# Optimization experiments

Measured on AMD Instinct MI355X. Metric: run time of the kernel, lower is better.

## Reference

```python
import jax, jax.numpy as jnp
import numpy as np


def setup_inputs() -> dict:
    key = jax.random.key(0)
    kY, kH = jax.random.split(key)
    B, M, L, S = 4, 512, 31, 2
    W = M + L - 1  # 542: dispersed measurement width
    Y = jax.random.uniform(kY, (B, M, W, S), dtype=jnp.float32)
    H = jax.random.uniform(kH, (B, M, M, L), dtype=jnp.float32)
    return {"Y": Y, "H": H}


def reference(Y, H):
    # Y: [B, M, W, S] measurement (W = M+L-1), H: [B, M, M, L] coded aperture
    B, M, W, S = Y.shape
    L = H.shape[-1]
    # tf.roll(Y, -i, axis=2)[:, :, 0:M] == Y[:, :, (j+i) % W] for j in [0, M)
    idx = (jnp.arange(M)[:, None] + jnp.arange(L)[None, :]) % W  # [M, L]
    Xs = Y[:, :, idx, :]                      # [B, M, M, L, S] shifted volume
    X = jnp.sum(H[..., None] * Xs, axis=4)    # sum over shots -> [B, M, M, L]
    return X / jnp.max(X)
```

## Files before the change

kernel.cpp:

```cpp
#include <hip/hip_runtime.h>

#define CB 4
#define CM 512
#define CL 31
#define CW 542
#define SLAB  (CM * CL)
#define SLAB4 (SLAB / 4)
#define NBM   (CB * CM)
#define CPAD  543


__device__ __forceinline__ void stage_ysum(const float* __restrict__ Y, int bm,
                                           float* __restrict__ ys) {
    const float2* y2 = (const float2*)(Y + (size_t)bm * (CW * 2));
    for (int j = threadIdx.x; j < CW; j += 256) {
        float2 v = y2[j];
        float s = v.x + v.y;
        ys[j]            = s;
        ys[j + CPAD]     = s;
        ys[j + 2 * CPAD] = s;
        ys[j + 3 * CPAD] = s;
    }
}

struct IdxState {
    int l0;
    int i0;
};

__device__ __forceinline__ IdxState idx_init(int tid) {
    unsigned f = 4u * (unsigned)tid;
    unsigned n = f / 31u;
    IdxState s;
    s.l0 = (int)(f - n * 31u);
    s.i0 = (int)n + s.l0;
    return s;
}

__device__ __forceinline__ void idx_quad(const IdxState& s,
                                         int& i0, int& i1, int& i2, int& i3) {
    i0 = s.i0;
    i1 = s.i0 + ((s.l0 >= 30) ? 1 - 30 : 1);
    i2 = s.i0 + ((s.l0 >= 29) ? 2 - 30 : 2);
    i3 = s.i0 + ((s.l0 >= 28) ? 3 - 30 : 3);
}

__device__ __forceinline__ void idx_step(IdxState& s) {
    bool w = (s.l0 == 30);
    s.i0 += w ? 4 : 34;
    s.l0  = w ? 0 : (s.l0 + 1);
}

__global__ __launch_bounds__(256, 8) void cassi_max(
    const float* __restrict__ Y,
    const float* __restrict__ H,
    float* __restrict__ blockmax)
{
    __shared__ float ysum[4 * CPAD];
    __shared__ float smax[4];
    const int bm  = blockIdx.x;
    const int tid = threadIdx.x;

    stage_ysum(Y, bm, ysum);
    __syncthreads();

    const float* ys = ysum + ((tid >> 3) & 3) * CPAD;
    const float4* h4 = (const float4*)(H + (size_t)bm * SLAB);

    IdxState st = idx_init(tid);
    float mx = 0.0f;

#pragma unroll 5
    for (int k = 0; k < 15; ++k) {
        float4 h = h4[tid + (k << 8)];
        int i0, i1, i2, i3;
        idx_quad(st, i0, i1, i2, i3);
        float v0 = h.x * ys[i0];
        float v1 = h.y * ys[i1];
        float v2 = h.z * ys[i2];
        float v3 = h.w * ys[i3];
        mx = fmaxf(mx, fmaxf(fmaxf(v0, v1), fmaxf(v2, v3)));
        idx_step(st);
    }
    if (tid < 128) {
        float4 h = h4[tid + 15 * 256];
        int i0, i1, i2, i3;
        idx_quad(st, i0, i1, i2, i3);
        float v0 = h.x * ys[i0];
        float v1 = h.y * ys[i1];
        float v2 = h.z * ys[i2];
        float v3 = h.w * ys[i3];
        mx = fmaxf(mx, fmaxf(fmaxf(v0, v1), fmaxf(v2, v3)));
    }

#pragma unroll
    for (int off = 32; off > 0; off >>= 1)
        mx = fmaxf(mx, __shfl_down(mx, off, 64));
    if ((tid & 63) == 0) smax[tid >> 6] = mx;
    __syncthreads();
    if (tid == 0)
        blockmax[bm] = fmaxf(fmaxf(smax[0], smax[1]), fmaxf(smax[2], smax[3]));
}

__global__ __launch_bounds__(256, 8) void cassi_out(
    const float* __restrict__ Y,
    const float* __restrict__ H,
    const float* __restrict__ blockmax,
    float* __restrict__ out)
{
    __shared__ float ysum[4 * CPAD];
    __shared__ float sm[4];
    const int bm  = blockIdx.x;
    const int tid = threadIdx.x;

    stage_ysum(Y, bm, ysum);

    float m = 0.0f;
    for (int j = tid; j < NBM; j += 256) m = fmaxf(m, blockmax[j]);
#pragma unroll
    for (int off = 32; off > 0; off >>= 1)
        m = fmaxf(m, __shfl_down(m, off, 64));
    if ((tid & 63) == 0) sm[tid >> 6] = m;
    __syncthreads();
    const float inv = 1.0f / fmaxf(fmaxf(sm[0], sm[1]), fmaxf(sm[2], sm[3]));

    const float* ys = ysum + ((tid >> 3) & 3) * CPAD;
    const float4* h4 = (const float4*)(H + (size_t)bm * SLAB);
    float4* o4 = (float4*)(out + (size_t)bm * SLAB);

    IdxState st = idx_init(tid);

#pragma unroll 5
    for (int k = 0; k < 15; ++k) {
        float4 h = h4[tid + (k << 8)];
        int i0, i1, i2, i3;
        idx_quad(st, i0, i1, i2, i3);
        float4 o;
        o.x = h.x * ys[i0] * inv;
        o.y = h.y * ys[i1] * inv;
        o.z = h.z * ys[i2] * inv;
        o.w = h.w * ys[i3] * inv;
        o4[tid + (k << 8)] = o;
        idx_step(st);
    }
    if (tid < 128) {
        float4 h = h4[tid + 15 * 256];
        int i0, i1, i2, i3;
        idx_quad(st, i0, i1, i2, i3);
        float4 o;
        o.x = h.x * ys[i0] * inv;
        o.y = h.y * ys[i1] * inv;
        o.z = h.z * ys[i2] * inv;
        o.w = h.w * ys[i3] * inv;
        o4[tid + 15 * 256] = o;
    }
}

extern "C" void kernel_launch(void* const* d_in, const int* in_sizes, int n_in,
                              void* d_out, int out_size, void* d_ws, size_t ws_size,
                              hipStream_t stream)
{
    const float* Y = (const float*)d_in[0];
    const float* H = (const float*)d_in[1];
    float* out = (float*)d_out;
    float* blockmax = (float*)d_ws;

    cassi_max<<<NBM, 256, 0, stream>>>(Y, H, blockmax);
    cassi_out<<<NBM, 256, 0, stream>>>(Y, H, blockmax, out);
}
```

Baseline: 259.5 us.

## Fuse max and scale passes into one cooperative kernel with grid sync

Merges the two launches into one cooperative kernel. Each block computes its slab max, a grid-wide sync makes every block max visible, and the block then rescales its own slab, keeping Y staging and possibly H in cache between phases. The second pass also uses nontemporal loads and stores. If the cooperative launch fails, it falls back to the two-kernel path. Risks are the cost of the grid barrier and the launch failing because 2048 blocks must all be resident at once.

```diff
diff --git a/kernel.cpp b/kernel.cpp
--- a/kernel.cpp
+++ b/kernel.cpp
@@ -1,4 +1,7 @@
 #include <hip/hip_runtime.h>
+#include <hip/hip_cooperative_groups.h>
+
+namespace cg = cooperative_groups;
 
 #define CB 4
 #define CM 512
@@ -8,6 +11,8 @@
 #define SLAB4 (SLAB / 4)
 #define NBM   (CB * CM)
 #define CPAD  543
+
+typedef float f32x4 __attribute__((ext_vector_type(4)));
 
 
 __device__ __forceinline__ void stage_ysum(const float* __restrict__ Y, int bm,
@@ -51,10 +56,74 @@
     s.l0  = w ? 0 : (s.l0 + 1);
 }
 
-__global__ __launch_bounds__(256, 8) void cassi_max(
+__device__ __forceinline__ float slab_max(const f32x4* __restrict__ h4,
+                                          const float* __restrict__ ys, int tid) {
+    IdxState st = idx_init(tid);
+    float mx = 0.0f;
+#pragma unroll 5
+    for (int k = 0; k < 15; ++k) {
+        f32x4 h = h4[tid + (k << 8)];
+        int i0, i1, i2, i3;
+        idx_quad(st, i0, i1, i2, i3);
+        mx = fmaxf(mx, fmaxf(fmaxf(h[0] * ys[i0], h[1] * ys[i1]),
+                             fmaxf(h[2] * ys[i2], h[3] * ys[i3])));
+        idx_step(st);
+    }
+    if (tid < 128) {
+        f32x4 h = h4[tid + 15 * 256];
+        int i0, i1, i2, i3;
+        idx_quad(st, i0, i1, i2, i3);
+        mx = fmaxf(mx, fmaxf(fmaxf(h[0] * ys[i0], h[1] * ys[i1]),
+                             fmaxf(h[2] * ys[i2], h[3] * ys[i3])));
+    }
+    return mx;
+}
+
+__device__ __forceinline__ void slab_scale(const f32x4* __restrict__ h4,
+                                           f32x4* __restrict__ o4,
+                                           const float* __restrict__ ys,
+                                           int tid, float inv) {
+    IdxState st = idx_init(tid);
+#pragma unroll 5
+    for (int k = 0; k < 15; ++k) {
+        f32x4 h = __builtin_nontemporal_load(&h4[tid + (k << 8)]);
+        int i0, i1, i2, i3;
+        idx_quad(st, i0, i1, i2, i3);
+        f32x4 o;
+        o[0] = h[0] * ys[i0] * inv;
+        o[1] = h[1] * ys[i1] * inv;
+        o[2] = h[2] * ys[i2] * inv;
+        o[3] = h[3] * ys[i3] * inv;
+        __builtin_nontemporal_store(o, &o4[tid + (k << 8)]);
+        idx_step(st);
+    }
+    if (tid < 128) {
+        f32x4 h = __builtin_nontemporal_load(&h4[tid + 15 * 256]);
+        int i0, i1, i2, i3;
+        idx_quad(st, i0, i1, i2, i3);
+        f32x4 o;
+        o[0] = h[0] * ys[i0] * inv;
+        o[1] = h[1] * ys[i1] * inv;
+        o[2] = h[2] * ys[i2] * inv;
+        o[3] = h[3] * ys[i3] * inv;
+        __builtin_nontemporal_store(o, &o4[tid + 15 * 256]);
+    }
+}
+
+__device__ __forceinline__ float block_reduce_max(float v, float* smax, int tid) {
+#pragma unroll
+    for (int off = 32; off > 0; off >>= 1)
+        v = fmaxf(v, __shfl_down(v, off, 64));
+    if ((tid & 63) == 0) smax[tid >> 6] = v;
+    __syncthreads();
+    return fmaxf(fmaxf(smax[0], smax[1]), fmaxf(smax[2], smax[3]));
+}
+
+__global__ __launch_bounds__(256, 8) void cassi_fused(
     const float* __restrict__ Y,
     const float* __restrict__ H,
-    float* __restrict__ blockmax)
+    float* __restrict__ blockmax,
+    float* __restrict__ out)
 {
     __shared__ float ysum[4 * CPAD];
     __shared__ float smax[4];
@@ -65,51 +134,49 @@
     __syncthreads();
 
     const float* ys = ysum + ((tid >> 3) & 3) * CPAD;
-    const float4* h4 = (const float4*)(H + (size_t)bm * SLAB);
-
-    IdxState st = idx_init(tid);
-    float mx = 0.0f;
-
-#pragma unroll 5
-    for (int k = 0; k < 15; ++k) {
-        float4 h = h4[tid + (k << 8)];
-        int i0, i1, i2, i3;
-        idx_quad(st, i0, i1, i2, i3);
-        float v0 = h.x * ys[i0];
-        float v1 = h.y * ys[i1];
-        float v2 = h.z * ys[i2];
-        float v3 = h.w * ys[i3];
-        mx = fmaxf(mx, fmaxf(fmaxf(v0, v1), fmaxf(v2, v3)));
-        idx_step(st);
-    }
-    if (tid < 128) {
-        float4 h = h4[tid + 15 * 256];
-        int i0, i1, i2, i3;
-        idx_quad(st, i0, i1, i2, i3);
-        float v0 = h.x * ys[i0];
-        float v1 = h.y * ys[i1];
-        float v2 = h.z * ys[i2];
-        float v3 = h.w * ys[i3];
-        mx = fmaxf(mx, fmaxf(fmaxf(v0, v1), fmaxf(v2, v3)));
-    }
-
-#pragma unroll
-    for (int off = 32; off > 0; off >>= 1)
-        mx = fmaxf(mx, __shfl_down(mx, off, 64));
-    if ((tid & 63) == 0) smax[tid >> 6] = mx;
-    __syncthreads();
-    if (tid == 0)
-        blockmax[bm] = fmaxf(fmaxf(smax[0], smax[1]), fmaxf(smax[2], smax[3]));
-}
-
-__global__ __launch_bounds__(256, 8) void cassi_out(
+    const f32x4* h4 = (const f32x4*)(H + (size_t)bm * SLAB);
+
+    float mx   = slab_max(h4, ys, tid);
+    float bmax = block_reduce_max(mx, smax, tid);
+    if (tid == 0) blockmax[bm] = bmax;
+
+    cg::this_grid().sync();
+
+    float m = 0.0f;
+    for (int j = tid; j < NBM; j += 256) m = fmaxf(m, blockmax[j]);
+    const float inv = 1.0f / block_reduce_max(m, smax, tid);
+
+    slab_scale(h4, (f32x4*)(out + (size_t)bm * SLAB), ys, tid, inv);
+}
+
+__global__ __launch_bounds__(256, 8) void cassi_max_k(
+    const float* __restrict__ Y,
+    const float* __restrict__ H,
+    float* __restrict__ blockmax)
+{
+    __shared__ float ysum[4 * CPAD];
+    __shared__ float smax[4];
+    const int bm  = blockIdx.x;
+    const int tid = threadIdx.x;
+
+    stage_ysum(Y, bm, ysum);
+    __syncthreads();
+
+    const float* ys = ysum + ((tid >> 3) & 3) * CPAD;
+    const f32x4* h4 = (const f32x4*)(H + (size_t)bm * SLAB);
+
+    float bmax = block_reduce_max(slab_max(h4, ys, tid), smax, tid);
+    if (tid == 0) blockmax[bm] = bmax;
+}
+
+__global__ __launch_bounds__(256, 8) void cassi_out_k(
     const float* __restrict__ Y,
     const float* __restrict__ H,
     const float* __restrict__ blockmax,
     float* __restrict__ out)
 {
     __shared__ float ysum[4 * CPAD];
-    __shared__ float sm[4];
+    __shared__ float smax[4];
     const int bm  = blockIdx.x;
     const int tid = threadIdx.x;
 
@@ -120,51 +187,30 @@
 #pragma unroll
     for (int off = 32; off > 0; off >>= 1)
         m = fmaxf(m, __shfl_down(m, off, 64));
-    if ((tid & 63) == 0) sm[tid >> 6] = m;
-    __syncthreads();
-    const float inv = 1.0f / fmaxf(fmaxf(sm[0], sm[1]), fmaxf(sm[2], sm[3]));
+    if ((tid & 63) == 0) smax[tid >> 6] = m;
+    __syncthreads();
+    const float inv = 1.0f / fmaxf(fmaxf(smax[0], smax[1]), fmaxf(smax[2], smax[3]));
 
     const float* ys = ysum + ((tid >> 3) & 3) * CPAD;
-    const float4* h4 = (const float4*)(H + (size_t)bm * SLAB);
-    float4* o4 = (float4*)(out + (size_t)bm * SLAB);
-
-    IdxState st = idx_init(tid);
-
-#pragma unroll 5
-    for (int k = 0; k < 15; ++k) {
-        float4 h = h4[tid + (k << 8)];
-        int i0, i1, i2, i3;
-        idx_quad(st, i0, i1, i2, i3);
-        float4 o;
-        o.x = h.x * ys[i0] * inv;
-        o.y = h.y * ys[i1] * inv;
-        o.z = h.z * ys[i2] * inv;
-        o.w = h.w * ys[i3] * inv;
-        o4[tid + (k << 8)] = o;
-        idx_step(st);
-    }
-    if (tid < 128) {
-        float4 h = h4[tid + 15 * 256];
-        int i0, i1, i2, i3;
-        idx_quad(st, i0, i1, i2, i3);
-        float4 o;
-        o.x = h.x * ys[i0] * inv;
-        o.y = h.y * ys[i1] * inv;
-        o.z = h.z * ys[i2] * inv;
-        o.w = h.w * ys[i3] * inv;
-        o4[tid + 15 * 256] = o;
-    }
+    const f32x4* h4 = (const f32x4*)(H + (size_t)bm * SLAB);
+    slab_scale(h4, (f32x4*)(out + (size_t)bm * SLAB), ys, tid, inv);
 }
 
 extern "C" void kernel_launch(void* const* d_in, const int* in_sizes, int n_in,
                               void* d_out, int out_size, void* d_ws, size_t ws_size,
                               hipStream_t stream)
 {
+    (void)in_sizes; (void)n_in; (void)out_size; (void)ws_size;
     const float* Y = (const float*)d_in[0];
     const float* H = (const float*)d_in[1];
     float* out = (float*)d_out;
     float* blockmax = (float*)d_ws;
 
-    cassi_max<<<NBM, 256, 0, stream>>>(Y, H, blockmax);
-    cassi_out<<<NBM, 256, 0, stream>>>(Y, H, blockmax, out);
-}
+    void* args[] = { (void*)&Y, (void*)&H, (void*)&blockmax, (void*)&out };
+    hipError_t err = hipLaunchCooperativeKernel((const void*)cassi_fused,
+                                                dim3(NBM), dim3(256), args, 0, stream);
+    if (err != hipSuccess) {
+        cassi_max_k<<<NBM, 256, 0, stream>>>(Y, H, blockmax);
+        cassi_out_k<<<NBM, 256, 0, stream>>>(Y, H, blockmax, out);
+    }
+}
```

Result: slower. 472.9 us (+82.2%).
